# Kernel tuning notes

Measured on AMD Instinct MI355X. Metric: run time of the kernel, lower is better.

The kernel has to match this reference:

```python
import jax, jax.numpy as jnp
import numpy as np

N = 4096        # num nodes
D = 512         # d_model (in_dim)
F = 512         # dff (out_dim)
H = 4           # num_heads
ALPHA = 0.3     # tf.keras LeakyReLU default


def setup_inputs() -> dict:
    key = jax.random.key(0)
    ks = jax.random.split(key, 9)
    s_in = 1.0 / np.sqrt(D)
    s_out = 1.0 / np.sqrt(F)
    return {
        "nodes": jax.random.normal(ks[0], (N, D), jnp.float32),
        "edges": jax.random.normal(ks[1], (N, D), jnp.float32),
        "labels": jax.random.normal(ks[2], (N, D), jnp.float32),
        # edge_layer Dense(dff)
        "We": jax.random.normal(ks[3], (D, F), jnp.float32) * s_in,
        "be": jnp.zeros((F,), jnp.float32),
        # per-head kernels stacked on leading head axis
        "W": jax.random.normal(ks[4], (H, D, F), jnp.float32) * s_in,
        "b": jax.random.normal(ks[5], (H, F), jnp.float32) * 0.01,
        "u": jax.random.normal(ks[6], (H, F), jnp.float32) * s_out,  # attn_kernel_self (squeezed)
        "v": jax.random.normal(ks[7], (H, F), jnp.float32) * s_out,  # attn_kernel_neighs (squeezed)
    }


def reference(nodes, edges, labels, We, be, W, b, u, v):
    # edge projection shared across heads: Dense(edges + labels)
    e = (edges + labels) @ We + be                       # [N, F]
    # per-head node projection: features = nodes @ W_h + b_h
    feats = jnp.einsum('nd,hdf->hnf', nodes, W) + b[:, None, :]   # [H, N, F]
    # rank-1 additive attention scores
    a_self = jnp.einsum('hnf,hf->hn', feats, u)          # [H, N]
    a_neigh = jnp.einsum('hnf,hf->hn', feats, v)         # [H, N]
    feats = feats + e[None]                              # [H, N, F]
    scores = a_self[:, :, None] * a_neigh[:, None, :]    # [H, N, N] outer product
    scores = jnp.where(scores >= 0, scores, ALPHA * scores)  # LeakyReLU(0.3)
    attn = jax.nn.softmax(scores, axis=-1)               # [H, N, N]
    out = jnp.einsum('hnm,hmf->hnf', attn, feats)        # [H, N, F]
    return jax.nn.relu(out.mean(axis=0))                 # [N, F]
```

## Files before the change

### kernel.cpp

```cpp
#include <hip/hip_runtime.h>

#define NN 4096
#define DD 512
#define FF 512
#define HH 4
#define KK 1024

typedef _Float16 f16;
typedef f16 f16x8 __attribute__((ext_vector_type(8)));
typedef f16 f16x4 __attribute__((ext_vector_type(4)));
typedef float f32x4 __attribute__((ext_vector_type(4)));
typedef float f32x16 __attribute__((ext_vector_type(16)));

typedef __attribute__((address_space(1))) void gvoid;
typedef __attribute__((address_space(3))) void svoid;
__device__ __forceinline__ void glds16(const void* g, void* s) {
    __builtin_amdgcn_global_load_lds((gvoid*)g, (svoid*)s, 16, 0, 0);
}

__device__ __attribute__((aligned(16))) f16 g_catA[NN * KK];
__device__ __attribute__((aligned(16))) f16 g_catB[HH * FF * KK];
__device__ __attribute__((aligned(16))) f16 g_featsH[HH * FF * NN];
__device__ __attribute__((aligned(16))) f16 g_oaccH[(size_t)2 * HH * NN * FF];
__device__ float g_Zp[2 * HH * NN];
__device__ float g_bcat[HH * FF];
__device__ float g_tu[HH * DD], g_tv[HH * DD], g_bu[HH], g_bv[HH];
__device__ float g_p[HH * NN], g_q[HH * NN];

#define PREP_CONV 4104
#define PREP_TRAN 320
#define PREP_UV   513

__global__ __launch_bounds__(256) void k_prep(const float* __restrict__ nodes, const float* __restrict__ edges,
                                              const float* __restrict__ labels, const float* __restrict__ We,
                                              const float* __restrict__ W, const float* __restrict__ be,
                                              const float* __restrict__ b, const float* __restrict__ u,
                                              const float* __restrict__ v) {
    __shared__ float lds[64 * 65];
    int bx = blockIdx.x;
    int tid = threadIdx.x;
    if (bx < PREP_CONV) {
        int id = bx * 256 + tid;
        const int NQ = NN * DD / 4;
        if (id < NQ) {
            f32x4 vv = *(const f32x4*)(nodes + (size_t)id * 4);
            f16x4 ov;
#pragma unroll
            for (int k = 0; k < 4; ++k) ov[k] = (f16)vv[k];
            *(f16x4*)&g_catA[(size_t)(id >> 7) * KK + (id & 127) * 4] = ov;
            return;
        }
        id -= NQ;
        if (id < NQ) {
            f32x4 ev = *(const f32x4*)(edges  + (size_t)id * 4);
            f32x4 lv = *(const f32x4*)(labels + (size_t)id * 4);
            f16x4 ov;
#pragma unroll
            for (int k = 0; k < 4; ++k) ov[k] = (f16)(ev[k] + lv[k]);
            *(f16x4*)&g_catA[(size_t)(id >> 7) * KK + 512 + (id & 127) * 4] = ov;
            return;
        }
        id -= NQ;
        if (id < HH * FF) { g_bcat[id] = b[id] + be[id & 511]; return; }
        return;
    }
    if (bx < PREP_CONV + PREP_TRAN) {
        int bid = bx - PREP_CONV;
        int mi = bid >> 6;
        int t64 = bid & 63;
        const float* src = (mi == 0) ? We : (W + (size_t)(mi - 1) * DD * FF);
        int ti = t64 >> 3, tj = t64 & 7;
        int r = tid >> 2, cseg = (tid & 3) * 16;
#pragma unroll
        for (int kq = 0; kq < 4; ++kq) {
            f32x4 vv = *(const f32x4*)(src + (size_t)(ti * 64 + r) * 512 + tj * 64 + cseg + kq * 4);
            *(f32x4*)&lds[r * 65 + cseg + kq * 4] = vv;
        }
        __syncthreads();
        int fl = tid >> 2, dseg = (tid & 3) * 16;
        f16x8 o0, o1;
#pragma unroll
        for (int k = 0; k < 8; ++k) o0[k] = (f16)lds[(dseg + k) * 65 + fl];
#pragma unroll
        for (int k = 0; k < 8; ++k) o1[k] = (f16)lds[(dseg + 8 + k) * 65 + fl];
        size_t frow = (size_t)(tj * 64 + fl);
        size_t dcol = (size_t)(ti * 64 + dseg);
        if (mi == 0) {
#pragma unroll
            for (int hh = 0; hh < HH; ++hh) {
                size_t ob = ((size_t)hh * FF + frow) * KK + 512 + dcol;
                *(f16x8*)&g_catB[ob] = o0;
                *(f16x8*)&g_catB[ob + 8] = o1;
            }
        } else {
            size_t ob = ((size_t)(mi - 1) * FF + frow) * KK + dcol;
            *(f16x8*)&g_catB[ob] = o0;
            *(f16x8*)&g_catB[ob + 8] = o1;
        }
        return;
    }
    {
        int row = (bx - PREP_CONV - PREP_TRAN) * 4 + (tid >> 6);
        int lane = tid & 63;
        float su = 0.f, sv = 0.f;
        if (row < HH * DD) {
            int h = row >> 9, d = row & 511;
            size_t wb = (size_t)h * DD * FF + (size_t)d * FF;
#pragma unroll
            for (int j = 0; j < 8; ++j) {
                int f = lane + 64 * j;
                float wv = W[wb + f];
                su += wv * u[(size_t)h * FF + f];
                sv += wv * v[(size_t)h * FF + f];
            }
        } else if (row < HH * DD + HH) {
            int h = row - HH * DD;
#pragma unroll
            for (int j = 0; j < 8; ++j) {
                int f = lane + 64 * j;
                float bvv = b[(size_t)h * FF + f];
                su += bvv * u[(size_t)h * FF + f];
                sv += bvv * v[(size_t)h * FF + f];
            }
        }
#pragma unroll
        for (int m = 1; m < 64; m <<= 1) {
            su += __shfl_xor(su, m, 64);
            sv += __shfl_xor(sv, m, 64);
        }
        if (lane == 0 && row < HH * DD + HH) {
            if (row < HH * DD) { g_tu[row] = su; g_tv[row] = sv; }
            else { g_bu[row - HH * DD] = su; g_bv[row - HH * DD] = sv; }
        }
    }
}

__global__ __launch_bounds__(256) void k_pq() {
    int row = blockIdx.x * 4 + (threadIdx.x >> 6);
    int lane = threadIdx.x & 63;
    int h = row >> 12, n = row & 4095;
    const f16* nb = g_catA + (size_t)n * KK + lane * 8;
    const float* tu = g_tu + h * DD + lane * 8;
    const float* tv = g_tv + h * DD + lane * 8;
    f16x8 nv8 = *(const f16x8*)nb;
    f32x4 tu0 = *(const f32x4*)tu, tu1 = *(const f32x4*)(tu + 4);
    f32x4 tv0 = *(const f32x4*)tv, tv1 = *(const f32x4*)(tv + 4);
    float pa = 0.f, qa = 0.f;
#pragma unroll
    for (int j = 0; j < 4; ++j) {
        float nv = (float)nv8[j];
        pa += nv * tu0[j];
        qa += nv * tv0[j];
    }
#pragma unroll
    for (int j = 0; j < 4; ++j) {
        float nv = (float)nv8[4 + j];
        pa += nv * tu1[j];
        qa += nv * tv1[j];
    }
#pragma unroll
    for (int m = 1; m < 64; m <<= 1) {
        pa += __shfl_xor(pa, m, 64);
        qa += __shfl_xor(qa, m, 64);
    }
    if (lane == 0) {
        g_p[row] = pa + g_bu[h];
        g_q[row] = qa + g_bv[h];
    }
}

__global__ __launch_bounds__(256, 2) void k_gemm_feats() {
    __shared__ f16 As[128 * 128];
    __shared__ f16 Bs[128 * 128];
    int tid = threadIdx.x;
    int lane = tid & 63, wave = tid >> 6;
    int wr = wave & 1, wc = wave >> 1;
    int c = lane & 15, g = lane >> 4;
    int n0 = blockIdx.x * 128, f0 = blockIdx.y * 128;
    int h = blockIdx.z;
    const f16* Bgl = g_catB + (size_t)h * FF * KK;
    int r4 = lane >> 4;
    int ch = lane & 15;
    f32x4 acc[4][4] = {};
    for (int kk = 0; kk < KK; kk += 128) {
        __syncthreads();
#pragma unroll
        for (int j = 0; j < 8; ++j) {
            int rowb = wave * 32 + j * 4;
            int row = rowb + r4;
            int src = (ch ^ (row & 15)) * 8;
            glds16(g_catA + (size_t)(n0 + row) * KK + kk + src, &As[rowb * 128]);
            glds16(Bgl    + (size_t)(f0 + row) * KK + kk + src, &Bs[rowb * 128]);
        }
        __syncthreads();
#pragma unroll
        for (int s = 0; s < 4; ++s) {
            f16x8 af[4], bf[4];
#pragma unroll
            for (int i = 0; i < 4; ++i) {
                int ra = wr * 64 + i * 16 + c;
                af[i] = *(const f16x8*)&As[ra * 128 + (((s * 4 + g) ^ (ra & 15)) * 8)];
            }
#pragma unroll
            for (int jj = 0; jj < 4; ++jj) {
                int rb = wc * 64 + jj * 16 + c;
                bf[jj] = *(const f16x8*)&Bs[rb * 128 + (((s * 4 + g) ^ (rb & 15)) * 8)];
            }
#pragma unroll
            for (int i = 0; i < 4; ++i)
#pragma unroll
                for (int jj = 0; jj < 4; ++jj)
                    acc[i][jj] = __builtin_amdgcn_mfma_f32_16x16x32_f16(af[i], bf[jj], acc[i][jj], 0, 0, 0);
        }
    }
#pragma unroll
    for (int jj = 0; jj < 4; ++jj) {
        int f = f0 + wc * 64 + jj * 16 + c;
        float bv = g_bcat[h * FF + f];
#pragma unroll
        for (int i = 0; i < 4; ++i) {
            int r0 = n0 + wr * 64 + i * 16 + g * 4;
            f16x4 ov;
#pragma unroll
            for (int rr = 0; rr < 4; ++rr) ov[rr] = (f16)(acc[i][jj][rr] + bv);
            *(f16x4*)(g_featsH + ((size_t)h * FF + f) * NN + r0) = ov;
        }
    }
}

#define WCALC(qv, dstvec, idx)                                              \
    {                                                                       \
        float s_ = pv * (qv);                                               \
        s_ = fmaxf(s_, 0.3f * s_);                                          \
        float e_ = __builtin_amdgcn_exp2f(__builtin_fmaf(s_, L2E, -mvb));   \
        zacc += e_;                                                         \
        dstvec[idx] = (f16)e_;                                              \
    }
#define GEN8(qa, qb, w)                                                     \
    {                                                                       \
        _Pragma("unroll") for (int k_ = 0; k_ < 4; ++k_) {                  \
            WCALC((qa)[k_], w, k_);                                         \
            WCALC((qb)[k_], w, 4 + k_);                                     \
        }                                                                   \
    }

__global__ __launch_bounds__(512, 2) void k_gemm_out() {
    __shared__ f16 As2[2][128 * 68];
    __shared__ float redmax[8], redmin[8];
    int tid = threadIdx.x;
    int lane = tid & 63, wave = tid >> 6;
    int wf = wave;
    int c5 = lane & 31, h5 = lane >> 5;
    int bid = blockIdx.x;
    int xcd = bid & 7;
    int h = xcd >> 1;
    int ks = xcd & 1;
    int n0 = (bid >> 3) * 128;
    int wn = tid >> 2, kq = (tid & 3) * 16;
    const float L2E = 1.44269504f;
    float pv = g_p[h * NN + n0 + wn];
    const float* qh = g_q + h * NN + ks * 2048;
    const f16* Bgl = g_featsH + (size_t)h * FF * NN + (size_t)ks * 2048;
    float mvb;
    {
        const float* qfull = g_q + h * NN + tid * 8;
        f32x4 a = *(const f32x4*)qfull, b2 = *(const f32x4*)(qfull + 4);
        float lmax = -1e30f, lmin = 1e30f;
#pragma unroll
        for (int j = 0; j < 4; ++j) {
            lmax = fmaxf(lmax, fmaxf(a[j], b2[j]));
            lmin = fminf(lmin, fminf(a[j], b2[j]));
        }
#pragma unroll
        for (int m = 1; m < 64; m <<= 1) {
            lmax = fmaxf(lmax, __shfl_xor(lmax, m, 64));
            lmin = fminf(lmin, __shfl_xor(lmin, m, 64));
        }
        if (lane == 0) { redmax[wave] = lmax; redmin[wave] = lmin; }
        __syncthreads();
        float qmax = redmax[0], qmin = redmin[0];
#pragma unroll
        for (int w2 = 1; w2 < 8; ++w2) {
            qmax = fmaxf(qmax, redmax[w2]);
            qmin = fminf(qmin, redmin[w2]);
        }
        float se = pv * (pv >= 0.f ? qmax : qmin);
        float Mv = fmaxf(se, 0.3f * se);
        mvb = Mv * L2E + 6.0f;
    }
    const f16* rowA = Bgl + (size_t)(wf * 64 + c5) * NN;
    const f16* rowB = Bgl + (size_t)(wf * 64 + 32 + c5) * NN;
    float zacc = 0.f;
    f32x16 acc[4][2] = {};
    f16x8 wA, wB;

    {
        const float* qp = qh + kq;
        f32x4 q0 = *(const f32x4*)qp, q1 = *(const f32x4*)(qp + 4),
              q2 = *(const f32x4*)(qp + 8), q3 = *(const f32x4*)(qp + 12);
        GEN8(q0, q1, wA);
        GEN8(q2, q3, wB);
        *(f16x8*)&As2[0][wn * 68 + kq] = wA;
        *(f16x8*)&As2[0][wn * 68 + kq + 8] = wB;
        const float* qp1 = qh + 64 + kq;
        q0 = *(const f32x4*)qp1; q1 = *(const f32x4*)(qp1 + 4);
        q2 = *(const f32x4*)(qp1 + 8); q3 = *(const f32x4*)(qp1 + 12);
        GEN8(q0, q1, wA);
        GEN8(q2, q3, wB);
    }
    __syncthreads();

    int cur = 0;
    for (int t = 0; t < 32; ++t) {
        if (t < 31) {
            int nxt = cur ^ 1;
            *(f16x8*)&As2[nxt][wn * 68 + kq] = wA;
            *(f16x8*)&As2[nxt][wn * 68 + kq + 8] = wB;
        }
        int mb = t * 64 + h5 * 8;
        f16x8 b00 = *(const f16x8*)(rowA + mb);
        f16x8 b01 = *(const f16x8*)(rowB + mb);
        f16x8 b10 = *(const f16x8*)(rowA + mb + 16);
        f16x8 b11 = *(const f16x8*)(rowB + mb + 16);
        f16x8 b20 = *(const f16x8*)(rowA + mb + 32);
        f16x8 b21 = *(const f16x8*)(rowB + mb + 32);
        f16x8 b30 = *(const f16x8*)(rowA + mb + 48);
        f16x8 b31 = *(const f16x8*)(rowB + mb + 48);
        f32x4 q0, q1, q2, q3;
        if (t < 30) {
            const float* qp = qh + t * 64 + 128 + kq;
            q0 = *(const f32x4*)qp; q1 = *(const f32x4*)(qp + 4);
            q2 = *(const f32x4*)(qp + 8); q3 = *(const f32x4*)(qp + 12);
        }
#pragma unroll
        for (int sk = 0; sk < 4; ++sk) {
            int cA = (sk * 2 + h5) * 8;
            f16x8 af0 = *(const f16x8*)&As2[cur][(c5) * 68 + cA];
            f16x8 af1 = *(const f16x8*)&As2[cur][(32 + c5) * 68 + cA];
            f16x8 af2 = *(const f16x8*)&As2[cur][(64 + c5) * 68 + cA];
            f16x8 af3 = *(const f16x8*)&As2[cur][(96 + c5) * 68 + cA];
            f16x8 bf0 = (sk == 0) ? b00 : (sk == 1) ? b10 : (sk == 2) ? b20 : b30;
            f16x8 bf1 = (sk == 0) ? b01 : (sk == 1) ? b11 : (sk == 2) ? b21 : b31;
            acc[0][0] = __builtin_amdgcn_mfma_f32_32x32x16_f16(af0, bf0, acc[0][0], 0, 0, 0);
            acc[0][1] = __builtin_amdgcn_mfma_f32_32x32x16_f16(af0, bf1, acc[0][1], 0, 0, 0);
            acc[1][0] = __builtin_amdgcn_mfma_f32_32x32x16_f16(af1, bf0, acc[1][0], 0, 0, 0);
            acc[1][1] = __builtin_amdgcn_mfma_f32_32x32x16_f16(af1, bf1, acc[1][1], 0, 0, 0);
            acc[2][0] = __builtin_amdgcn_mfma_f32_32x32x16_f16(af2, bf0, acc[2][0], 0, 0, 0);
            acc[2][1] = __builtin_amdgcn_mfma_f32_32x32x16_f16(af2, bf1, acc[2][1], 0, 0, 0);
            acc[3][0] = __builtin_amdgcn_mfma_f32_32x32x16_f16(af3, bf0, acc[3][0], 0, 0, 0);
            acc[3][1] = __builtin_amdgcn_mfma_f32_32x32x16_f16(af3, bf1, acc[3][1], 0, 0, 0);
            if (t < 30) {
                if (sk == 1) { GEN8(q0, q1, wA); }
                if (sk == 2) { GEN8(q2, q3, wB); }
            }
        }
        __syncthreads();
        cur ^= 1;
    }
    zacc += __shfl_xor(zacc, 1, 64);
    zacc += __shfl_xor(zacc, 2, 64);
    if ((tid & 3) == 0) g_Zp[(size_t)(h * 2 + ks) * NN + n0 + wn] = zacc;
    f16* O = g_oaccH + (size_t)(h * 2 + ks) * NN * FF;
#pragma unroll
    for (int it = 0; it < 4; ++it)
#pragma unroll
        for (int jt = 0; jt < 2; ++jt) {
            int f = wf * 64 + jt * 32 + c5;
#pragma unroll
            for (int qd = 0; qd < 4; ++qd) {
                int r0 = n0 + it * 32 + qd * 8 + h5 * 4;
#pragma unroll
                for (int rr = 0; rr < 4; ++rr)
                    O[(size_t)(r0 + rr) * FF + f] = (f16)acc[it][jt][qd * 4 + rr];
            }
        }
}

__global__ void k_reduce(float* __restrict__ out) {
    int t = blockIdx.x * 256 + threadIdx.x;
    size_t i = (size_t)t * 8;
    int n = t >> 6;
    const size_t NF = (size_t)NN * FF;
    float s[8] = {0.f, 0.f, 0.f, 0.f, 0.f, 0.f, 0.f, 0.f};
#pragma unroll
    for (int h = 0; h < HH; ++h) {
        float Z = g_Zp[(size_t)(2 * h) * NN + n] + g_Zp[(size_t)(2 * h + 1) * NN + n];
        float sc = 0.25f / Z;
        f16x8 a = *(const f16x8*)(g_oaccH + (size_t)(2 * h) * NF + i);
        f16x8 bsl = *(const f16x8*)(g_oaccH + (size_t)(2 * h + 1) * NF + i);
#pragma unroll
        for (int rr = 0; rr < 8; ++rr) s[rr] += ((float)a[rr] + (float)bsl[rr]) * sc;
    }
    f32x4 o0, o1;
#pragma unroll
    for (int rr = 0; rr < 4; ++rr) o0[rr] = fmaxf(s[rr], 0.f);
#pragma unroll
    for (int rr = 0; rr < 4; ++rr) o1[rr] = fmaxf(s[4 + rr], 0.f);
    *(f32x4*)(out + i) = o0;
    *(f32x4*)(out + i + 4) = o1;
}

extern "C" void kernel_launch(void* const* d_in, const int* in_sizes, int n_in,
                              void* d_out, int out_size, void* d_ws, size_t ws_size,
                              hipStream_t stream) {
    (void)in_sizes; (void)n_in; (void)out_size; (void)d_ws; (void)ws_size;
    const float* nodes  = (const float*)d_in[0];
    const float* edges  = (const float*)d_in[1];
    const float* labels = (const float*)d_in[2];
    const float* We     = (const float*)d_in[3];
    const float* be     = (const float*)d_in[4];
    const float* W      = (const float*)d_in[5];
    const float* b      = (const float*)d_in[6];
    const float* u      = (const float*)d_in[7];
    const float* v      = (const float*)d_in[8];

    k_prep<<<PREP_CONV + PREP_TRAN + PREP_UV, 256, 0, stream>>>(nodes, edges, labels, We, W, be, b, u, v);
    k_pq<<<4096, 256, 0, stream>>>();
    k_gemm_feats<<<dim3(32, 4, 4), 256, 0, stream>>>();
    k_gemm_out<<<256, 512, 0, stream>>>();
    k_reduce<<<1024, 256, 0, stream>>>((float*)d_out);
}
```

Before: 224.4 us.

## Shrink attention-output GEMM tile to 64 rows by half F with 256-thread blocks

Measured after the change: 278.5 us. +24.1%, slower.

```diff
diff --git a/kernel.cpp b/kernel.cpp
--- a/kernel.cpp
+++ b/kernel.cpp
@@ -243,19 +243,31 @@
             WCALC((qb)[k_], w, 4 + k_);                                     \
         }                                                                   \
     }
-
-__global__ __launch_bounds__(512, 2) void k_gemm_out() {
-    __shared__ f16 As2[2][128 * 68];
-    __shared__ float redmax[8], redmin[8];
+#define SKSTEP(skidx, bfa, bfb)                                             \
+    {                                                                       \
+        int cA_ = ((skidx) * 2 + h5) * 8;                                   \
+        f16x8 af0 = *(const f16x8*)&As2[cur][(c5) * 68 + cA_];              \
+        f16x8 af1 = *(const f16x8*)&As2[cur][(32 + c5) * 68 + cA_];         \
+        acc[0][0] = __builtin_amdgcn_mfma_f32_32x32x16_f16(af0, bfa, acc[0][0], 0, 0, 0); \
+        acc[0][1] = __builtin_amdgcn_mfma_f32_32x32x16_f16(af0, bfb, acc[0][1], 0, 0, 0); \
+        acc[1][0] = __builtin_amdgcn_mfma_f32_32x32x16_f16(af1, bfa, acc[1][0], 0, 0, 0); \
+        acc[1][1] = __builtin_amdgcn_mfma_f32_32x32x16_f16(af1, bfb, acc[1][1], 0, 0, 0); \
+    }
+
+__global__ __launch_bounds__(256, 3) void k_gemm_out() {
+    __shared__ f16 As2[2][64 * 68];
+    __shared__ float redmax[4], redmin[4];
     int tid = threadIdx.x;
     int lane = tid & 63, wave = tid >> 6;
-    int wf = wave;
     int c5 = lane & 31, h5 = lane >> 5;
     int bid = blockIdx.x;
     int xcd = bid & 7;
     int h = xcd >> 1;
     int ks = xcd & 1;
-    int n0 = (bid >> 3) * 128;
+    int r = bid >> 3;
+    int fh = r & 1;
+    int n0 = (r >> 1) * 64;
+    int fb = fh * 256;
     int wn = tid >> 2, kq = (tid & 3) * 16;
     const float L2E = 1.44269504f;
     float pv = g_p[h * NN + n0 + wn];
@@ -263,13 +275,16 @@
     const f16* Bgl = g_featsH + (size_t)h * FF * NN + (size_t)ks * 2048;
     float mvb;
     {
-        const float* qfull = g_q + h * NN + tid * 8;
-        f32x4 a = *(const f32x4*)qfull, b2 = *(const f32x4*)(qfull + 4);
+        const float* qfull = g_q + h * NN + tid * 16;
         float lmax = -1e30f, lmin = 1e30f;
 #pragma unroll
         for (int j = 0; j < 4; ++j) {
-            lmax = fmaxf(lmax, fmaxf(a[j], b2[j]));
-            lmin = fminf(lmin, fminf(a[j], b2[j]));
+            f32x4 a = *(const f32x4*)(qfull + j * 4);
+#pragma unroll
+            for (int k = 0; k < 4; ++k) {
+                lmax = fmaxf(lmax, a[k]);
+                lmin = fminf(lmin, a[k]);
+            }
         }
 #pragma unroll
         for (int m = 1; m < 64; m <<= 1) {
@@ -280,7 +295,7 @@
         __syncthreads();
         float qmax = redmax[0], qmin = redmin[0];
 #pragma unroll
-        for (int w2 = 1; w2 < 8; ++w2) {
+        for (int w2 = 1; w2 < 4; ++w2) {
             qmax = fmaxf(qmax, redmax[w2]);
             qmin = fminf(qmin, redmin[w2]);
         }
@@ -288,10 +303,10 @@
         float Mv = fmaxf(se, 0.3f * se);
         mvb = Mv * L2E + 6.0f;
     }
-    const f16* rowA = Bgl + (size_t)(wf * 64 + c5) * NN;
-    const f16* rowB = Bgl + (size_t)(wf * 64 + 32 + c5) * NN;
+    const f16* rowA = Bgl + (size_t)(fb + wave * 64 + c5) * NN;
+    const f16* rowB = rowA + (size_t)32 * NN;
     float zacc = 0.f;
-    f32x16 acc[4][2] = {};
+    f32x16 acc[2][2] = {};
     f16x8 wA, wB;
 
     {
@@ -312,48 +327,31 @@
 
     int cur = 0;
     for (int t = 0; t < 32; ++t) {
-        if (t < 31) {
-            int nxt = cur ^ 1;
-            *(f16x8*)&As2[nxt][wn * 68 + kq] = wA;
-            *(f16x8*)&As2[nxt][wn * 68 + kq + 8] = wB;
-        }
         int mb = t * 64 + h5 * 8;
         f16x8 b00 = *(const f16x8*)(rowA + mb);
         f16x8 b01 = *(const f16x8*)(rowB + mb);
         f16x8 b10 = *(const f16x8*)(rowA + mb + 16);
         f16x8 b11 = *(const f16x8*)(rowB + mb + 16);
-        f16x8 b20 = *(const f16x8*)(rowA + mb + 32);
-        f16x8 b21 = *(const f16x8*)(rowB + mb + 32);
-        f16x8 b30 = *(const f16x8*)(rowA + mb + 48);
-        f16x8 b31 = *(const f16x8*)(rowB + mb + 48);
+        if (t < 31) {
+            int nxt = cur ^ 1;
+            *(f16x8*)&As2[nxt][wn * 68 + kq] = wA;
+            *(f16x8*)&As2[nxt][wn * 68 + kq + 8] = wB;
+        }
         f32x4 q0, q1, q2, q3;
         if (t < 30) {
             const float* qp = qh + t * 64 + 128 + kq;
             q0 = *(const f32x4*)qp; q1 = *(const f32x4*)(qp + 4);
             q2 = *(const f32x4*)(qp + 8); q3 = *(const f32x4*)(qp + 12);
         }
-#pragma unroll
-        for (int sk = 0; sk < 4; ++sk) {
-            int cA = (sk * 2 + h5) * 8;
-            f16x8 af0 = *(const f16x8*)&As2[cur][(c5) * 68 + cA];
-            f16x8 af1 = *(const f16x8*)&As2[cur][(32 + c5) * 68 + cA];
-            f16x8 af2 = *(const f16x8*)&As2[cur][(64 + c5) * 68 + cA];
-            f16x8 af3 = *(const f16x8*)&As2[cur][(96 + c5) * 68 + cA];
-            f16x8 bf0 = (sk == 0) ? b00 : (sk == 1) ? b10 : (sk == 2) ? b20 : b30;
-            f16x8 bf1 = (sk == 0) ? b01 : (sk == 1) ? b11 : (sk == 2) ? b21 : b31;
-            acc[0][0] = __builtin_amdgcn_mfma_f32_32x32x16_f16(af0, bf0, acc[0][0], 0, 0, 0);
-            acc[0][1] = __builtin_amdgcn_mfma_f32_32x32x16_f16(af0, bf1, acc[0][1], 0, 0, 0);
-            acc[1][0] = __builtin_amdgcn_mfma_f32_32x32x16_f16(af1, bf0, acc[1][0], 0, 0, 0);
-            acc[1][1] = __builtin_amdgcn_mfma_f32_32x32x16_f16(af1, bf1, acc[1][1], 0, 0, 0);
-            acc[2][0] = __builtin_amdgcn_mfma_f32_32x32x16_f16(af2, bf0, acc[2][0], 0, 0, 0);
-            acc[2][1] = __builtin_amdgcn_mfma_f32_32x32x16_f16(af2, bf1, acc[2][1], 0, 0, 0);
-            acc[3][0] = __builtin_amdgcn_mfma_f32_32x32x16_f16(af3, bf0, acc[3][0], 0, 0, 0);
-            acc[3][1] = __builtin_amdgcn_mfma_f32_32x32x16_f16(af3, bf1, acc[3][1], 0, 0, 0);
-            if (t < 30) {
-                if (sk == 1) { GEN8(q0, q1, wA); }
-                if (sk == 2) { GEN8(q2, q3, wB); }
-            }
-        }
+        SKSTEP(0, b00, b01);
+        SKSTEP(1, b10, b11);
+        f16x8 b20 = *(const f16x8*)(rowA + mb + 32);
+        f16x8 b21 = *(const f16x8*)(rowB + mb + 32);
+        f16x8 b30 = *(const f16x8*)(rowA + mb + 48);
+        f16x8 b31 = *(const f16x8*)(rowB + mb + 48);
+        if (t < 30) { GEN8(q0, q1, wA); GEN8(q2, q3, wB); }
+        SKSTEP(2, b20, b21);
+        SKSTEP(3, b30, b31);
         __syncthreads();
         cur ^= 1;
     }
@@ -362,10 +360,10 @@
     if ((tid & 3) == 0) g_Zp[(size_t)(h * 2 + ks) * NN + n0 + wn] = zacc;
     f16* O = g_oaccH + (size_t)(h * 2 + ks) * NN * FF;
 #pragma unroll
-    for (int it = 0; it < 4; ++it)
+    for (int it = 0; it < 2; ++it)
 #pragma unroll
         for (int jt = 0; jt < 2; ++jt) {
-            int f = wf * 64 + jt * 32 + c5;
+            int f = fb + wave * 64 + jt * 32 + c5;
 #pragma unroll
             for (int qd = 0; qd < 4; ++qd) {
                 int r0 = n0 + it * 32 + qd * 8 + h5 * 4;
@@ -417,6 +415,6 @@
     k_prep<<<PREP_CONV + PREP_TRAN + PREP_UV, 256, 0, stream>>>(nodes, edges, labels, We, W, be, b, u, v);
     k_pq<<<4096, 256, 0, stream>>>();
     k_gemm_feats<<<dim3(32, 4, 4), 256, 0, stream>>>();
-    k_gemm_out<<<256, 512, 0, stream>>>();
+    k_gemm_out<<<1024, 256, 0, stream>>>();
     k_reduce<<<1024, 256, 0, stream>>>((float*)d_out);
 }
```
